# Performance work log

Hardware: AMD Instinct MI355X
Metric: run time of the kernel (lower is better)

The kernel has to match this reference:

```python
import jax, jax.numpy as jnp
import numpy as np

BATCH = 2      # batch_size (number of videos)
NUM_HEADS = 8


def setup_inputs() -> dict:
    key = jax.random.key(0)
    k1, k2, k3 = jax.random.split(key, 3)
    B, H, W, C = 16, 64, 64, 512
    return {
        "hidden_states": jax.random.normal(k1, (B, H, W, C), dtype=jnp.float32),
        "w_qkv": jax.random.normal(k2, (3 * C, C), dtype=jnp.float32) * (C ** -0.5),
        "b_qkv": jax.random.normal(k3, (3 * C,), dtype=jnp.float32) * 0.02,
    }


def reference(hidden_states, w_qkv, b_qkv):
    B, H, W, C = hidden_states.shape
    bs, nh = BATCH, NUM_HEADS
    f = B // bs                      # video_length
    hd = C // nh                     # head_dim
    scale = hd ** -0.5

    # qkv projection (torch Linear: x @ W.T + b)
    qkv = hidden_states @ w_qkv.T + b_qkv                       # [B,H,W,3C]
    qkv = qkv.reshape(B, H * W, 3, nh, hd)
    qkv = qkv.transpose(2, 0, 3, 1, 4).reshape(3, B * nh, H * W, hd)
    q, k, v = qkv[0], qkv[1], qkv[2]                            # [B*nh, HW, hd]

    # NOTE: original rearrange labels '(b n f)' but memory layout is (b f) n;
    # it is a pure reshape, so replicate as flat reshape (faithful to math).
    q = q.reshape(bs, nh, f, H, W, hd)
    k = k.reshape(bs, nh, f, H, W, hd)
    v = v.reshape(bs, nh, f, H, W, hd)

    # q cat is identity; k/v: prepend last frame == cyclic roll by +1 on frames
    k = jnp.roll(k, 1, axis=2)
    v = jnp.roll(v, 1, axis=2)

    q = q.reshape(bs, nh, f, H * W, hd)
    # faithful flat reshape (scrambles (h,w,c) -> (hd, HW) order, as in torch)
    k = k.reshape(bs, nh, f, hd, H * W)
    v = v.reshape(bs, nh, f, H * W, hd)

    # einsums with NO contracted index: elementwise-transpose products
    attn = jnp.einsum('bnfhw,bnfwh->bnhfw', q * scale, k)       # [bs,nh,HW,f,hd]
    attn = jax.nn.softmax(attn, axis=-1)
    x = jnp.einsum('bnhfw,bnfhw->bnhfw', attn, v)               # [bs,nh,HW,f,hd]

    # faithful flat reshape (torch .view on contiguous tensor)
    x = x.reshape(bs, nh, f, H, W, hd)
    # rearrange 'b n f h w c -> (b f) h w (n c)'
    x = x.transpose(0, 2, 3, 4, 1, 5).reshape(bs * f, H, W, nh * hd)
    return x
```

## Files before the change

kernel.cpp:

```cpp
#include <hip/hip_runtime.h>
#include <math.h>


typedef _Float16 half8 __attribute__((ext_vector_type(8)));
typedef _Float16 half4 __attribute__((ext_vector_type(4)));
typedef __fp16 fp16x2 __attribute__((ext_vector_type(2)));
typedef float f32x4 __attribute__((ext_vector_type(4)));

__device__ __forceinline__ half8 pk8(const float4 x, const float4 y) {
    fp16x2 a = __builtin_amdgcn_cvt_pkrtz(x.x, x.y);
    fp16x2 b = __builtin_amdgcn_cvt_pkrtz(x.z, x.w);
    fp16x2 c = __builtin_amdgcn_cvt_pkrtz(y.x, y.y);
    fp16x2 d = __builtin_amdgcn_cvt_pkrtz(y.z, y.w);
    half8 r;
    r[0] = (_Float16)a[0]; r[1] = (_Float16)a[1];
    r[2] = (_Float16)b[0]; r[3] = (_Float16)b[1];
    r[4] = (_Float16)c[0]; r[5] = (_Float16)c[1];
    r[6] = (_Float16)d[0]; r[7] = (_Float16)d[1];
    return r;
}

__device__ __forceinline__ void gload_lds16(const void* g, void* l) {
    __builtin_amdgcn_global_load_lds(
        (const __attribute__((address_space(1))) unsigned int*)g,
        (__attribute__((address_space(3))) unsigned int*)l, 16, 0, 0);
}

__global__ __launch_bounds__(256) void cvt_fp16(
    const float* __restrict__ src, _Float16* __restrict__ dst)
{
    const size_t i = (size_t)blockIdx.x * 256 + threadIdx.x;
    const float4 x = *reinterpret_cast<const float4*>(src + i * 8);
    const float4 y = *reinterpret_cast<const float4*>(src + i * 8 + 4);
    *reinterpret_cast<half8*>(dst + i * 8) = pk8(x, y);
}

__global__ __launch_bounds__(256) void cvt_w_frag(
    const float* __restrict__ W, _Float16* __restrict__ Wf)
{
    const int gid  = blockIdx.x * 256 + threadIdx.x;
    const int lane = gid & 63;
    const int nf   = (gid >> 6) & 3;
    const int ks   = (gid >> 8) & 15;
    const int ntw  = gid >> 12;
    const float* src =
        W + (size_t)(ntw * 64 + nf * 16 + (lane & 15)) * 512 +
        ks * 32 + (lane >> 4) * 8;
    const float4 x = *reinterpret_cast<const float4*>(src);
    const float4 y = *reinterpret_cast<const float4*>(src + 4);
    *reinterpret_cast<half8*>(Wf + (size_t)gid * 8) = pk8(x, y);
}

__global__ __launch_bounds__(256, 4) void gemm_qkv_wf(
    const _Float16* __restrict__ Ah, const _Float16* __restrict__ Wf,
    const float* __restrict__ bias, _Float16* __restrict__ C)
{
    __shared__ __align__(16) _Float16 lds[9216];

    const int lin = blockIdx.x;
    const int swz = (lin & 7) * 768 + (lin >> 3);
    const int nt = swz % 12, mt = swz / 12;
    const int row0 = mt * 128, col0 = nt * 128;

    const int tid = threadIdx.x, wid = tid >> 6, lane = tid & 63;
    const int wm = wid >> 1, wn = wid & 1, l15 = lane & 15, kq = lane >> 4;

    const int s0  = wid * 2;
    const int rA0 = s0 * 16 + (lane >> 2);
    const int rA1 = rA0 + 16;
    const int c0  = (lane & 3) ^ ((rA0 >> 1) & 3);
    const int c1  = (lane & 3) ^ ((rA1 >> 1) & 3);
    const _Float16* ga0 = Ah + (size_t)(row0 + rA0) * 512 + c0 * 8;
    const _Float16* ga1 = Ah + (size_t)(row0 + rA1) * 512 + c1 * 8;

    const _Float16* wfb = Wf + (size_t)(nt * 2 + wn) * 32768 + lane * 8;

    f32x4 acc[4][4];
#pragma unroll
    for (int i = 0; i < 4; ++i)
#pragma unroll
        for (int j = 0; j < 4; ++j) acc[i][j] = (f32x4)0.f;

    half8 wfa[4], wfb_[4];

#define STAGE_A(KB, BUF)                                                       \
    do {                                                                       \
        _Float16* bdst = lds + (BUF) * 4096;                                   \
        gload_lds16(ga0 + (KB), bdst + s0 * 512);                              \
        gload_lds16(ga1 + (KB), bdst + (s0 + 1) * 512);                        \
    } while (0)

#define LOAD_W(DST, KS)                                                        \
    do {                                                                       \
        _Pragma("unroll")                                                      \
        for (int nf = 0; nf < 4; ++nf)                                         \
            DST[nf] = *reinterpret_cast<const half8*>(                         \
                wfb + (KS) * 2048 + nf * 512);                                 \
    } while (0)

#define FRAG_MFMA(BC, WU)                                                      \
    do {                                                                       \
        half8 ah[4];                                                           \
        _Pragma("unroll")                                                      \
        for (int mf = 0; mf < 4; ++mf) {                                       \
            const int r  = wm * 64 + mf * 16 + l15;                            \
            const int ph = (kq ^ ((r >> 1) & 3)) * 8;                          \
            ah[mf] = *reinterpret_cast<const half8*>((BC) + r * 32 + ph);      \
        }                                                                      \
        _Pragma("unroll")                                                      \
        for (int nf = 0; nf < 4; ++nf)                                         \
            _Pragma("unroll")                                                  \
            for (int mf = 0; mf < 4; ++mf)                                     \
                acc[mf][nf] = __builtin_amdgcn_mfma_f32_16x16x32_f16(          \
                    ah[mf], WU[nf], acc[mf][nf], 0, 0, 0);                     \
    } while (0)

#define BARRIER()                                                              \
    do {                                                                       \
        asm volatile("s_waitcnt vmcnt(0) lgkmcnt(0)" ::: "memory");            \
        __builtin_amdgcn_sched_barrier(0);                                     \
        __builtin_amdgcn_s_barrier();                                          \
        __builtin_amdgcn_sched_barrier(0);                                     \
    } while (0)

#define STEP(T, WU, WL)                                                        \
    do {                                                                       \
        const int kn1 = ((T) + 1 < 16) ? (T) + 1 : 15;                         \
        STAGE_A(kn1 * 32, ((T) + 1) & 1);                                      \
        LOAD_W(WL, kn1);                                                       \
        FRAG_MFMA(lds + ((T) & 1) * 4096, WU);                                 \
        BARRIER();                                                             \
    } while (0)

    STAGE_A(0, 0);
    LOAD_W(wfa, 0);
    BARRIER();

#pragma unroll 1
    for (int t = 0; t < 16; t += 2) {
        STEP(t,     wfa, wfb_);
        STEP(t + 1, wfb_, wfa);
    }
#undef STEP
#undef BARRIER
#undef FRAG_MFMA
#undef LOAD_W
#undef STAGE_A

    float* wbase = reinterpret_cast<float*>(lds) + wid * 1088;
    const float4 bv4 = *reinterpret_cast<const float4*>(
        &bias[col0 + wn * 64 + l15 * 4]);

#pragma unroll
    for (int mf = 0; mf < 4; ++mf) {
#pragma unroll
        for (int nf = 0; nf < 4; ++nf)
#pragma unroll
            for (int j = 0; j < 4; ++j)
                wbase[(kq * 4 + j) * 68 + nf * 16 + l15] = acc[mf][nf][j];
        __syncthreads();
#pragma unroll
        for (int i = 0; i < 4; ++i) {
            const int r16 = i * 4 + kq;
            float4 v = *reinterpret_cast<float4*>(wbase + r16 * 68 + l15 * 4);
            half4 h;
            h[0] = (_Float16)(v.x + bv4.x);
            h[1] = (_Float16)(v.y + bv4.y);
            h[2] = (_Float16)(v.z + bv4.z);
            h[3] = (_Float16)(v.w + bv4.w);
            const int r = row0 + wm * 64 + mf * 16 + r16;
            *reinterpret_cast<half4*>(
                &C[(size_t)r * 1536 + col0 + wn * 64 + l15 * 4]) = h;
        }
        __syncthreads();
    }
}

__global__ __launch_bounds__(256) void attn_scramble(
    const _Float16* __restrict__ qkv, float* __restrict__ out)
{
    __shared__ float Ks[64][68];
    const int bid = blockIdx.x;
    const int hw6 = bid & 63;
    const int n   = (bid >> 6) & 7;
    const int b   = bid >> 9;
    const int kn  = (n + 7) & 7;
    const int t   = threadIdx.x;
    {
        const int lx = t & 7;
        const int rp = t >> 3;
#pragma unroll
        for (int p = 0; p < 2; ++p) {
            const int dp = p * 32 + rp;
            const half8 kv = *reinterpret_cast<const half8*>(
                &qkv[(size_t)(b * 4096 + dp * 64 + hw6) * 1536 + 512 +
                     kn * 64 + lx * 8]);
#pragma unroll
            for (int e = 0; e < 8; ++e)
                Ks[lx * 8 + e][dp] = (float)kv[e];
        }
    }
    __syncthreads();
    const int row = t >> 2;
    const int tl  = t & 3;
    const size_t rbase = (size_t)(b * 4096 + hw6 * 64 + row) * 1536;
    float s[16];
    {
        const _Float16* qp = qkv + rbase + n * 64 + tl * 16;
        const half8 q0 = *reinterpret_cast<const half8*>(qp);
        const half8 q1 = *reinterpret_cast<const half8*>(qp + 8);
        float q[16], kk[16];
#pragma unroll
        for (int e = 0; e < 8; ++e) {
            q[e] = (float)q0[e];
            q[8 + e] = (float)q1[e];
        }
#pragma unroll
        for (int u = 0; u < 4; ++u)
            *reinterpret_cast<float4*>(&kk[u * 4]) =
                *reinterpret_cast<const float4*>(&Ks[row][tl * 16 + u * 4]);
        float m = -1e30f;
#pragma unroll
        for (int u = 0; u < 16; ++u) {
            s[u] = 0.125f * q[u] * kk[u];
            m = fmaxf(m, s[u]);
        }
        m = fmaxf(m, __shfl_xor(m, 1));
        m = fmaxf(m, __shfl_xor(m, 2));
        float sum = 0.f;
#pragma unroll
        for (int u = 0; u < 16; ++u) {
            s[u] = __expf(s[u] - m);
            sum += s[u];
        }
        sum += __shfl_xor(sum, 1);
        sum += __shfl_xor(sum, 2);
        const float inv = 1.0f / sum;
#pragma unroll
        for (int u = 0; u < 16; ++u) s[u] *= inv;
    }
    const _Float16* vp = qkv + rbase + 1024 + kn * 64 + tl * 16;
    const half8 v0 = *reinterpret_cast<const half8*>(vp);
    const half8 v1 = *reinterpret_cast<const half8*>(vp + 8);
    const int vb = b >> 3, fr = b & 7;
    float* op = out +
        ((size_t)(((vb * 8 + (hw6 >> 3)) * 64 + ((hw6 & 7) * 8 + (row >> 3))) * 64 +
                  ((row & 7) * 8 + n)) * 512) + fr * 64 + tl * 16;
    float4 o0, o1, o2, o3;
    o0.x = s[0]  * (float)v0[0]; o0.y = s[1]  * (float)v0[1];
    o0.z = s[2]  * (float)v0[2]; o0.w = s[3]  * (float)v0[3];
    o1.x = s[4]  * (float)v0[4]; o1.y = s[5]  * (float)v0[5];
    o1.z = s[6]  * (float)v0[6]; o1.w = s[7]  * (float)v0[7];
    o2.x = s[8]  * (float)v1[0]; o2.y = s[9]  * (float)v1[1];
    o2.z = s[10] * (float)v1[2]; o2.w = s[11] * (float)v1[3];
    o3.x = s[12] * (float)v1[4]; o3.y = s[13] * (float)v1[5];
    o3.z = s[14] * (float)v1[6]; o3.w = s[15] * (float)v1[7];
    *reinterpret_cast<float4*>(op)      = o0;
    *reinterpret_cast<float4*>(op + 4)  = o1;
    *reinterpret_cast<float4*>(op + 8)  = o2;
    *reinterpret_cast<float4*>(op + 12) = o3;
}

extern "C" void kernel_launch(void* const* d_in, const int* in_sizes, int n_in,
                              void* d_out, int out_size, void* d_ws, size_t ws_size,
                              hipStream_t stream) {
    const float* hs = (const float*)d_in[0];
    const float* w  = (const float*)d_in[1];
    const float* bq = (const float*)d_in[2];
    float* out = (float*)d_out;
    _Float16* qkv = (_Float16*)d_ws;

    _Float16* Asp = (_Float16*)d_out;
    _Float16* Wf  = Asp + 33554432;

    cvt_fp16<<<16384, 256, 0, stream>>>(hs, Asp);
    cvt_w_frag<<<384, 256, 0, stream>>>(w, Wf);
    gemm_qkv_wf<<<6144, 256, 0, stream>>>(Asp, Wf, bq, qkv);
    attn_scramble<<<8192, 256, 0, stream>>>(qkv, out);
}
```

Measured before the change: 238.7 us.

## Load GEMM A fragments directly from global into registers, dropping LDS staging

The QKV projection GEMM no longer stages the A tile in LDS through global_load_lds with block barriers. Each wave now loads its A and W fragments straight from global memory into registers, double-buffered across k-steps, and raises wave priority around the MFMA bursts. This removes barrier synchronisation and LDS traffic from the main loop. In exchange, the two waves that share each A row block each read it from global/L2 separately, register pressure rises (launch bounds drop to 3 blocks per CU), and the A loads are only 16 bytes per lane with a stride of one row.

```diff
diff --git a/kernel.cpp b/kernel.cpp
--- a/kernel.cpp
+++ b/kernel.cpp
@@ -20,12 +20,6 @@
     return r;
 }
 
-__device__ __forceinline__ void gload_lds16(const void* g, void* l) {
-    __builtin_amdgcn_global_load_lds(
-        (const __attribute__((address_space(1))) unsigned int*)g,
-        (__attribute__((address_space(3))) unsigned int*)l, 16, 0, 0);
-}
-
 __global__ __launch_bounds__(256) void cvt_fp16(
     const float* __restrict__ src, _Float16* __restrict__ dst)
 {
@@ -51,11 +45,11 @@
     *reinterpret_cast<half8*>(Wf + (size_t)gid * 8) = pk8(x, y);
 }
 
-__global__ __launch_bounds__(256, 4) void gemm_qkv_wf(
+__global__ __launch_bounds__(256, 3) void gemm_nolds(
     const _Float16* __restrict__ Ah, const _Float16* __restrict__ Wf,
     const float* __restrict__ bias, _Float16* __restrict__ C)
 {
-    __shared__ __align__(16) _Float16 lds[9216];
+    __shared__ __align__(16) float eplds[4352];
 
     const int lin = blockIdx.x;
     const int swz = (lin & 7) * 768 + (lin >> 3);
@@ -65,15 +59,11 @@
     const int tid = threadIdx.x, wid = tid >> 6, lane = tid & 63;
     const int wm = wid >> 1, wn = wid & 1, l15 = lane & 15, kq = lane >> 4;
 
-    const int s0  = wid * 2;
-    const int rA0 = s0 * 16 + (lane >> 2);
-    const int rA1 = rA0 + 16;
-    const int c0  = (lane & 3) ^ ((rA0 >> 1) & 3);
-    const int c1  = (lane & 3) ^ ((rA1 >> 1) & 3);
-    const _Float16* ga0 = Ah + (size_t)(row0 + rA0) * 512 + c0 * 8;
-    const _Float16* ga1 = Ah + (size_t)(row0 + rA1) * 512 + c1 * 8;
-
-    const _Float16* wfb = Wf + (size_t)(nt * 2 + wn) * 32768 + lane * 8;
+    const _Float16* pA0 = Ah + (size_t)(row0 + wm * 64 +  0 + l15) * 512 + kq * 8;
+    const _Float16* pA1 = Ah + (size_t)(row0 + wm * 64 + 16 + l15) * 512 + kq * 8;
+    const _Float16* pA2 = Ah + (size_t)(row0 + wm * 64 + 32 + l15) * 512 + kq * 8;
+    const _Float16* pA3 = Ah + (size_t)(row0 + wm * 64 + 48 + l15) * 512 + kq * 8;
+    const _Float16* pW  = Wf + (size_t)(nt * 2 + wn) * 32768 + lane * 8;
 
     f32x4 acc[4][4];
 #pragma unroll
@@ -81,73 +71,51 @@
 #pragma unroll
         for (int j = 0; j < 4; ++j) acc[i][j] = (f32x4)0.f;
 
-    half8 wfa[4], wfb_[4];
-
-#define STAGE_A(KB, BUF)                                                       \
+    half8 aA[4], aB[4], wA[4], wB[4];
+
+#define LOADA(DST, T)                                                          \
     do {                                                                       \
-        _Float16* bdst = lds + (BUF) * 4096;                                   \
-        gload_lds16(ga0 + (KB), bdst + s0 * 512);                              \
-        gload_lds16(ga1 + (KB), bdst + (s0 + 1) * 512);                        \
+        DST[0] = *reinterpret_cast<const half8*>(pA0 + (T) * 32);              \
+        DST[1] = *reinterpret_cast<const half8*>(pA1 + (T) * 32);              \
+        DST[2] = *reinterpret_cast<const half8*>(pA2 + (T) * 32);              \
+        DST[3] = *reinterpret_cast<const half8*>(pA3 + (T) * 32);              \
     } while (0)
 
-#define LOAD_W(DST, KS)                                                        \
+#define LOADW(DST, T)                                                          \
     do {                                                                       \
-        _Pragma("unroll")                                                      \
-        for (int nf = 0; nf < 4; ++nf)                                         \
-            DST[nf] = *reinterpret_cast<const half8*>(                         \
-                wfb + (KS) * 2048 + nf * 512);                                 \
+        DST[0] = *reinterpret_cast<const half8*>(pW + (T) * 2048 +    0);      \
+        DST[1] = *reinterpret_cast<const half8*>(pW + (T) * 2048 +  512);      \
+        DST[2] = *reinterpret_cast<const half8*>(pW + (T) * 2048 + 1024);      \
+        DST[3] = *reinterpret_cast<const half8*>(pW + (T) * 2048 + 1536);      \
     } while (0)
 
-#define FRAG_MFMA(BC, WU)                                                      \
+#define FRAG(AS, WS)                                                           \
     do {                                                                       \
-        half8 ah[4];                                                           \
-        _Pragma("unroll")                                                      \
-        for (int mf = 0; mf < 4; ++mf) {                                       \
-            const int r  = wm * 64 + mf * 16 + l15;                            \
-            const int ph = (kq ^ ((r >> 1) & 3)) * 8;                          \
-            ah[mf] = *reinterpret_cast<const half8*>((BC) + r * 32 + ph);      \
-        }                                                                      \
+        __builtin_amdgcn_s_setprio(1);                                         \
         _Pragma("unroll")                                                      \
         for (int nf = 0; nf < 4; ++nf)                                         \
             _Pragma("unroll")                                                  \
             for (int mf = 0; mf < 4; ++mf)                                     \
                 acc[mf][nf] = __builtin_amdgcn_mfma_f32_16x16x32_f16(          \
-                    ah[mf], WU[nf], acc[mf][nf], 0, 0, 0);                     \
+                    AS[mf], WS[nf], acc[mf][nf], 0, 0, 0);                     \
+        __builtin_amdgcn_s_setprio(0);                                         \
     } while (0)
 
-#define BARRIER()                                                              \
-    do {                                                                       \
-        asm volatile("s_waitcnt vmcnt(0) lgkmcnt(0)" ::: "memory");            \
-        __builtin_amdgcn_sched_barrier(0);                                     \
-        __builtin_amdgcn_s_barrier();                                          \
-        __builtin_amdgcn_sched_barrier(0);                                     \
-    } while (0)
-
-#define STEP(T, WU, WL)                                                        \
-    do {                                                                       \
-        const int kn1 = ((T) + 1 < 16) ? (T) + 1 : 15;                         \
-        STAGE_A(kn1 * 32, ((T) + 1) & 1);                                      \
-        LOAD_W(WL, kn1);                                                       \
-        FRAG_MFMA(lds + ((T) & 1) * 4096, WU);                                 \
-        BARRIER();                                                             \
-    } while (0)
-
-    STAGE_A(0, 0);
-    LOAD_W(wfa, 0);
-    BARRIER();
-
-#pragma unroll 1
+    LOADA(aA, 0); LOADW(wA, 0);
+    LOADA(aB, 1); LOADW(wB, 1);
+
+#pragma unroll
     for (int t = 0; t < 16; t += 2) {
-        STEP(t,     wfa, wfb_);
-        STEP(t + 1, wfb_, wfa);
-    }
-#undef STEP
-#undef BARRIER
-#undef FRAG_MFMA
-#undef LOAD_W
-#undef STAGE_A
-
-    float* wbase = reinterpret_cast<float*>(lds) + wid * 1088;
+        FRAG(aA, wA);
+        if (t + 2 < 16) { LOADA(aA, t + 2); LOADW(wA, t + 2); }
+        FRAG(aB, wB);
+        if (t + 3 < 16) { LOADA(aB, t + 3); LOADW(wB, t + 3); }
+    }
+#undef FRAG
+#undef LOADW
+#undef LOADA
+
+    float* wbase = eplds + wid * 1088;
     const float4 bv4 = *reinterpret_cast<const float4*>(
         &bias[col0 + wn * 64 + l15 * 4]);
 
@@ -275,6 +243,6 @@
 
     cvt_fp16<<<16384, 256, 0, stream>>>(hs, Asp);
     cvt_w_frag<<<384, 256, 0, stream>>>(w, Wf);
-    gemm_qkv_wf<<<6144, 256, 0, stream>>>(Asp, Wf, bq, qkv);
+    gemm_nolds<<<6144, 256, 0, stream>>>(Asp, Wf, bq, qkv);
     attn_scramble<<<8192, 256, 0, stream>>>(qkv, out);
 }
```

After: 333.9 us. +39.9%, slower.
